# Performance work log

Measured on AMD Instinct MI355X. Metric: run time of the kernel, lower is better.

The kernel has to match this reference:

```python
import jax, jax.numpy as jnp
import numpy as np

N = 20000      # nodes
K = 32         # avg degree
E = N * K      # edges
H = 128        # num_hidden
NV = 128       # num_V
NE = 128       # num_E
NH = 4         # num_heads (hard-coded in module)
D = H // NH    # per-head dim


def setup_inputs() -> dict:
    key = jax.random.key(0)
    ks = jax.random.split(key, 16)
    w = lambda k, shape: jax.random.normal(k, shape, jnp.float32) * 0.02
    return {
        "h_V": jax.random.normal(ks[0], (N, NV), jnp.float32),
        "h_E": jax.random.normal(ks[1], (E, NE), jnp.float32),
        "edge_idx": jax.random.randint(ks[2], (2, E), 0, N, dtype=jnp.int64),
        # W_V: Linear(num_E, num_hidden) + GELU
        "Wv_w": w(ks[3], (H, NE)), "Wv_b": jnp.zeros((H,), jnp.float32),
        # Bias MLP: Linear(2*num_V+num_E, H) -> ReLU -> Linear(H, H) -> ReLU -> Linear(H, NH)
        "B1_w": w(ks[4], (H, 2 * NV + NE)), "B1_b": jnp.zeros((H,), jnp.float32),
        "B2_w": w(ks[5], (H, H)), "B2_b": jnp.zeros((H,), jnp.float32),
        "B3_w": w(ks[6], (NH, H)), "B3_b": jnp.zeros((NH,), jnp.float32),
        # W_O: Linear(H, num_V, bias=False); gate: Linear(H, num_V)
        "Wo_w": w(ks[7], (NV, H)),
        "gate_w": w(ks[8], (NV, H)), "gate_b": jnp.zeros((NV,), jnp.float32),
    }


def reference(h_V, h_E, edge_idx, Wv_w, Wv_b, B1_w, B1_b, B2_w, B2_b, B3_w, B3_b, Wo_w, gate_w, gate_b):
    src = edge_idx[0]
    dst = edge_idx[1]
    num_nodes = h_V.shape[0]

    # per-edge attention logits via small MLP on [h_V[src], h_E, h_V[dst]]
    cat = jnp.concatenate([h_V[src], h_E, h_V[dst]], axis=-1)          # [E, 2*NV+NE]
    x = jax.nn.relu(cat @ B1_w.T + B1_b)
    x = jax.nn.relu(x @ B2_w.T + B2_b)
    logits = (x @ B3_w.T + B3_b) / np.float32(np.sqrt(D))              # [E, NH]

    # per-edge values
    V = jax.nn.gelu(h_E @ Wv_w.T + Wv_b, approximate=False)           # [E, H]
    V = V.reshape(-1, NH, D)                                           # [E, NH, D]

    # scatter_softmax over edges grouped by src node
    m = jax.ops.segment_max(logits, src, num_segments=num_nodes)       # [N, NH]
    ex = jnp.exp(logits - m[src])                                      # [E, NH]
    denom = jax.ops.segment_sum(ex, src, num_segments=num_nodes)      # [N, NH]
    attend = ex / denom[src]                                           # [E, NH]

    # weighted scatter-sum aggregation
    agg = jax.ops.segment_sum(attend[:, :, None] * V, src, num_segments=num_nodes)
    agg = agg.reshape(num_nodes, -1)                                   # [N, H]

    h_V_gate = jax.nn.sigmoid(agg @ gate_w.T + gate_b)                 # [N, NV]
    dh = (agg @ Wo_w.T) * h_V_gate                                     # [N, NV]
    return h_V + dh
```

## Files before the change

### kernel.cpp

```cpp
#include <hip/hip_runtime.h>
#include <math.h>

typedef __attribute__((ext_vector_type(8))) short bf16x8;
typedef __attribute__((ext_vector_type(4))) float f32x4;
typedef unsigned short u16;

__device__ __forceinline__ short f2bf(float x) {
  union { float f; unsigned u; } c; c.f = x;
  unsigned u = c.u;
  u += 0x7fffu + ((u >> 16) & 1u);
  return (short)(u >> 16);
}
__device__ __forceinline__ float bf2f(u16 b) {
  union { unsigned u; float f; } c; c.u = ((unsigned)b) << 16; return c.f;
}
__device__ __forceinline__ unsigned pack2(float a, float b) {
  return ((unsigned)(u16)f2bf(a)) | (((unsigned)(u16)f2bf(b)) << 16);
}
__device__ __forceinline__ unsigned cvtpk(float lo, float hi) {
  unsigned r;
  asm("v_cvt_pk_bf16_f32 %0, %1, %2" : "=v"(r) : "v"(lo), "v"(hi));
  return r;
}
__device__ __forceinline__ float fast_erf(float x) {
  float ax = fabsf(x);
  float t = __frcp_rn(1.f + 0.3275911f * ax);
  float p = ((((1.061405429f * t - 1.453152027f) * t) + 1.421413741f) * t - 0.284496736f) * t + 0.254829592f;
  float y = 1.f - p * t * __expf(-ax * ax);
  return copysignf(y, x);
}
__device__ __forceinline__ void gload16(const void* g, void* l) {
  __builtin_amdgcn_global_load_lds(
      (const __attribute__((address_space(1))) void*)g,
      (__attribute__((address_space(3))) void*)l, 16, 0, 0);
}

__global__ void detect_kernel(const unsigned* __restrict__ idx32, int* __restrict__ flag) {
  __shared__ int anyNZ;
  if (threadIdx.x == 0) anyNZ = 0;
  __syncthreads();
  unsigned v = idx32[threadIdx.x * 2 + 1];
  if (v != 0u) atomicOr(&anyNZ, 1);
  __syncthreads();
  if (threadIdx.x == 0) *flag = (anyNZ == 0) ? 1 : 0;
}

__global__ void convert_count_kernel(const void* __restrict__ in, int* __restrict__ s32,
                                     const int* __restrict__ flag, int* __restrict__ cnt,
                                     int E) {
  int i = blockIdx.x * 256 + threadIdx.x;
  if (i >= 2 * E) return;
  int f = *flag;
  int v = f ? (int)((const long long*)in)[i] : ((const int*)in)[i];
  s32[i] = v;
  if (i < E) atomicAdd(&cnt[v], 1);
}

__global__ void __launch_bounds__(1024)
scan_kernel(const int* __restrict__ cnt, int* __restrict__ offs, int n) {
  __shared__ int sp[1024];
  int t = threadIdx.x;
  int chunk = (n + 1023) / 1024;
  int begin = t * chunk;
  int end = begin + chunk; if (end > n) end = n; if (begin > n) begin = n;
  int s = 0;
  for (int i = begin; i < end; ++i) s += cnt[i];
  sp[t] = s;
  __syncthreads();
  for (int o = 1; o < 1024; o <<= 1) {
    int v = (t >= o) ? sp[t - o] : 0;
    __syncthreads();
    sp[t] += v;
    __syncthreads();
  }
  int run = (t == 0) ? 0 : sp[t - 1];
  for (int i = begin; i < end; ++i) { offs[i] = run; run += cnt[i]; }
  if (t == 0) offs[n] = sp[1023];
}

__global__ void scatter_kernel(const int* __restrict__ src, const int* __restrict__ offs,
                               int* __restrict__ cur, int* __restrict__ order, int E) {
  int i = blockIdx.x * 256 + threadIdx.x;
  if (i >= E) return;
  int s = src[i];
  int p = offs[s] + atomicAdd(&cur[s], 1);
  order[p] = i;
}

__global__ void wcvt_kernel(const float* __restrict__ B1, const float* __restrict__ B2,
                            const float* __restrict__ B3, const float* __restrict__ Wv,
                            const float* __restrict__ Wo, const float* __restrict__ Wg,
                            short* __restrict__ o) {
  int i = blockIdx.x * 256 + threadIdx.x;
  if (i >= 115200) return;
  float val; int dst;
  if (i < 49152) {
    int row = i / 384, k = i % 384;
    val = B1[i];
    int c = k >> 5, s = (k >> 3) & 3, e = k & 7;
    dst = c * 4096 + row * 32 + ((s ^ ((row >> 1) & 3)) << 3) + e;
  } else if (i < 65536) {
    int j = i - 49152; int row = j >> 7, k = j & 127;
    val = B2[j];
    int c = k >> 5, s = (k >> 3) & 3, e = k & 7;
    dst = 49152 + c * 4096 + row * 32 + ((s ^ ((row >> 1) & 3)) << 3) + e;
  } else if (i < 66048) { val = B3[i - 65536]; dst = i; }
  else if (i < 82432) {
    int j = i - 66048; int row = j >> 7, k = j & 127;
    val = Wv[j];
    int c = k >> 5, s = (k >> 3) & 3, e = k & 7;
    dst = 66048 + c * 4096 + row * 32 + ((s ^ ((row >> 1) & 3)) << 3) + e;
  }
  else if (i < 98816)  { val = Wo[i - 82432]; dst = i; }
  else                 { val = Wg[i - 98816]; dst = i; }
  o[dst] = f2bf(val);
}

__global__ void cvtbf_kernel(const float* __restrict__ in, u16* __restrict__ out, long n8) {
  long i = (long)blockIdx.x * blockDim.x + threadIdx.x;
  long stride = (long)gridDim.x * blockDim.x;
  for (; i < n8; i += stride) {
    long b = i * 8;
    float4 a = *(const float4*)(in + b);
    float4 c = *(const float4*)(in + b + 4);
    uint4 u;
    u.x = pack2(a.x, a.y); u.y = pack2(a.z, a.w);
    u.z = pack2(c.x, c.y); u.w = pack2(c.z, c.w);
    *(uint4*)(out + b) = u;
  }
}

__global__ void __launch_bounds__(256, 3)
edge_kernel(const u16* __restrict__ hVb, const float* __restrict__ hE,
            const int* __restrict__ src, const int* __restrict__ dst,
            u16* __restrict__ Vout,
            const short* __restrict__ W1, const float* __restrict__ b1,
            const short* __restrict__ W2, const float* __restrict__ b2,
            const short* __restrict__ W3b, const float* __restrict__ b3,
            const short* __restrict__ Wv, const float* __restrict__ bv,
            float* __restrict__ logits, int E) {
  __shared__ u16 sE[64 * 128];
  __shared__ u16 sH[64 * 128];
  __shared__ u16 sW[2][4096];
  __shared__ float sPart[64][4][2];

  const int t = threadIdx.x;
  const int eBase = blockIdx.x * 64;
  const int lane = t & 63;
  const int wid = t >> 6;
  const int wrow = (wid >> 1) * 32;
  const int wcol = (wid & 1) * 64;
  const int lrow = lane & 15;
  const int kgrp = lane >> 4;

  auto STAGE = [&](const short* cp, int buf) {
#pragma unroll
    for (int i = 0; i < 2; ++i) {
      int L = t + i * 256;
      gload16(cp + L * 8, &sW[buf][L * 8]);
    }
  };

  STAGE(W1, 0);

#pragma unroll
  for (int i = 0; i < 4; ++i) {
    int u = t + i * 256;
    int row = u >> 4, sg = u & 15;
    const float* p = hE + (size_t)min(eBase + row, E - 1) * 128 + sg * 8;
    float4 f0 = *(const float4*)p;
    float4 f1 = *(const float4*)(p + 4);
    uint4 cv;
    cv.x = cvtpk(f0.x, f0.y); cv.y = cvtpk(f0.z, f0.w);
    cv.z = cvtpk(f1.x, f1.y); cv.w = cvtpk(f1.z, f1.w);
    *(uint4*)&sE[row * 128 + ((sg ^ (row & 15)) * 8)] = cv;
  }

  bf16x8 aS[4][2], aD[4][2];
  {
    int rS[2], rD[2];
#pragma unroll
    for (int mi = 0; mi < 2; ++mi) {
      int e = min(eBase + wrow + mi * 16 + lrow, E - 1);
      rS[mi] = src[e];
      rD[mi] = dst[e];
    }
#pragma unroll
    for (int c4 = 0; c4 < 4; ++c4) {
      const int kk = c4 * 32 + kgrp * 8;
#pragma unroll
      for (int mi = 0; mi < 2; ++mi) {
        aS[c4][mi] = *(const bf16x8*)(hVb + (size_t)rS[mi] * 128 + kk);
        aD[c4][mi] = *(const bf16x8*)(hVb + (size_t)rD[mi] * 128 + kk);
      }
    }
  }
  asm volatile("s_waitcnt vmcnt(0)" ::: "memory");
  __syncthreads();

  f32x4 acc[2][4];
  auto ZACC = [&]() {
#pragma unroll
    for (int mi = 0; mi < 2; ++mi)
#pragma unroll
      for (int nf = 0; nf < 4; ++nf)
#pragma unroll
        for (int q = 0; q < 4; ++q) acc[mi][nf][q] = 0.f;
  };
  auto LDSA = [&](const u16* s, int kk, bf16x8* a) {
#pragma unroll
    for (int mi = 0; mi < 2; ++mi) {
      int row = wrow + mi * 16 + lrow;
      int seg = (kk >> 3) ^ (row & 15);
      a[mi] = *(const bf16x8*)&s[row * 128 + seg * 8];
    }
  };
  auto STEP = [&](int buf, const short* nextCp, const bf16x8* a) {
    if (nextCp) STAGE(nextCp, buf ^ 1);
    bf16x8 b[4];
#pragma unroll
    for (int nf = 0; nf < 4; ++nf) {
      int row = wcol + nf * 16 + lrow;
      int seg = kgrp ^ ((row >> 1) & 3);
      b[nf] = *(const bf16x8*)&sW[buf][row * 32 + seg * 8];
    }
#pragma unroll
    for (int nf = 0; nf < 4; ++nf)
#pragma unroll
      for (int mi = 0; mi < 2; ++mi)
        acc[mi][nf] = __builtin_amdgcn_mfma_f32_16x16x32_bf16(a[mi], b[nf], acc[mi][nf], 0, 0, 0);
    if (nextCp) asm volatile("s_waitcnt vmcnt(0)" ::: "memory");
    __syncthreads();
  };

  ZACC();
  STEP(0, W1 + 1 * 4096, aS[0]);
  STEP(1, W1 + 2 * 4096, aS[1]);
  STEP(0, W1 + 3 * 4096, aS[2]);
  STEP(1, W1 + 4 * 4096, aS[3]);
#pragma unroll
  for (int c4 = 0; c4 < 4; ++c4) {
    bf16x8 a[2];
    LDSA(sE, c4 * 32 + kgrp * 8, a);
    STEP((4 + c4) & 1, W1 + (5 + c4) * 4096, a);
  }
  STEP(0, W1 + 9 * 4096, aD[0]);
  STEP(1, W1 + 10 * 4096, aD[1]);
  STEP(0, W1 + 11 * 4096, aD[2]);
  STEP(1, Wv, aD[3]);
  {
    float b1c[4];
#pragma unroll
    for (int nf = 0; nf < 4; ++nf) b1c[nf] = b1[wcol + nf * 16 + lrow];
#pragma unroll
    for (int mi = 0; mi < 2; ++mi)
#pragma unroll
      for (int nf = 0; nf < 4; ++nf)
#pragma unroll
        for (int q = 0; q < 4; ++q) {
          int row = wrow + mi * 16 + kgrp * 4 + q;
          int col = wcol + nf * 16 + lrow;
          int seg = (col >> 3) ^ (row & 15);
          sH[row * 128 + seg * 8 + (col & 7)] =
              (u16)f2bf(fmaxf(acc[mi][nf][q] + b1c[nf], 0.f));
        }
  }

  ZACC();
#pragma unroll
  for (int v = 0; v < 4; ++v) {
    bf16x8 a[2];
    LDSA(sE, v * 32 + kgrp * 8, a);
    const short* nxt = (v < 3) ? (Wv + (v + 1) * 4096) : W2;
    STEP(v & 1, nxt, a);
  }
  {
    float bvc[4];
#pragma unroll
    for (int nf = 0; nf < 4; ++nf) bvc[nf] = bv[wcol + nf * 16 + lrow];
#pragma unroll
    for (int mi = 0; mi < 2; ++mi)
#pragma unroll
      for (int nf = 0; nf < 4; ++nf)
#pragma unroll
        for (int q = 0; q < 4; ++q) {
          int row = wrow + mi * 16 + kgrp * 4 + q;
          int col = wcol + nf * 16 + lrow;
          float x = acc[mi][nf][q] + bvc[nf];
          float g = 0.5f * x * (1.0f + fast_erf(x * 0.70710678118654752f));
          int seg = (col >> 3) ^ (row & 15);
          sE[row * 128 + seg * 8 + (col & 7)] = (u16)f2bf(g);
        }
  }
  __syncthreads();
#pragma unroll
  for (int i = 0; i < 4; ++i) {
    int u = t + i * 256;
    int row = u >> 4, g16 = u & 15;
    int seg = g16 ^ (row & 15);
    uint4 v = *(const uint4*)&sE[row * 128 + seg * 8];
    int e = eBase + row;
    if (e < E) *(uint4*)(Vout + (size_t)e * 128 + g16 * 8) = v;
  }

  ZACC();
#pragma unroll
  for (int u = 0; u < 4; ++u) {
    bf16x8 a[2];
    LDSA(sH, u * 32 + kgrp * 8, a);
    const short* nxt = (u < 3) ? (W2 + (u + 1) * 4096) : nullptr;
    STEP(u & 1, nxt, a);
  }
  {
    float b2c[4], w3v[4][4];
#pragma unroll
    for (int nf = 0; nf < 4; ++nf) {
      int col = wcol + nf * 16 + lrow;
      b2c[nf] = b2[col];
#pragma unroll
      for (int h = 0; h < 4; ++h) w3v[h][nf] = bf2f((u16)W3b[h * 128 + col]);
    }
#pragma unroll
    for (int mi = 0; mi < 2; ++mi)
#pragma unroll
      for (int q = 0; q < 4; ++q) {
        float p0 = 0.f, p1 = 0.f, p2 = 0.f, p3 = 0.f;
#pragma unroll
        for (int nf = 0; nf < 4; ++nf) {
          float x = fmaxf(acc[mi][nf][q] + b2c[nf], 0.f);
          p0 += x * w3v[0][nf]; p1 += x * w3v[1][nf];
          p2 += x * w3v[2][nf]; p3 += x * w3v[3][nf];
        }
#pragma unroll
        for (int o = 1; o < 16; o <<= 1) {
          p0 += __shfl_xor(p0, o); p1 += __shfl_xor(p1, o);
          p2 += __shfl_xor(p2, o); p3 += __shfl_xor(p3, o);
        }
        if (lrow < 4) {
          float pw = (lrow == 0) ? p0 : (lrow == 1) ? p1 : (lrow == 2) ? p2 : p3;
          sPart[wrow + mi * 16 + kgrp * 4 + q][lrow][wid & 1] = pw;
        }
      }
  }
  __syncthreads();
  if (t < 64) {
    int e = eBase + t;
    if (e < E) {
      float4 lg;
      lg.x = (sPart[t][0][0] + sPart[t][0][1] + b3[0]) * 0.17677669529663687f;
      lg.y = (sPart[t][1][0] + sPart[t][1][1] + b3[1]) * 0.17677669529663687f;
      lg.z = (sPart[t][2][0] + sPart[t][2][1] + b3[2]) * 0.17677669529663687f;
      lg.w = (sPart[t][3][0] + sPart[t][3][1] + b3[3]) * 0.17677669529663687f;
      *(float4*)(logits + (size_t)e * 4) = lg;
    }
  }
}

__global__ void __launch_bounds__(256)
nm_kernel(const float* __restrict__ logits, const int* __restrict__ offs,
          const int* __restrict__ order, float* __restrict__ attw,
          float* __restrict__ inv, int nN) {
  const int wid = threadIdx.x >> 6, lane = threadIdx.x & 63;
  const int nW = gridDim.x * 4;
  for (int v = blockIdx.x * 4 + wid; v < nN; v += nW) {
    const int base = offs[v];
    const int deg = offs[v + 1] - base;
    float m0 = -3e38f, m1 = -3e38f, m2 = -3e38f, m3 = -3e38f;
    for (int i = lane; i < deg; i += 64) {
      int e = order[base + i];
      float4 l = *(const float4*)(logits + (size_t)e * 4);
      m0 = fmaxf(m0, l.x); m1 = fmaxf(m1, l.y);
      m2 = fmaxf(m2, l.z); m3 = fmaxf(m3, l.w);
    }
#pragma unroll
    for (int o = 32; o > 0; o >>= 1) {
      m0 = fmaxf(m0, __shfl_xor(m0, o)); m1 = fmaxf(m1, __shfl_xor(m1, o));
      m2 = fmaxf(m2, __shfl_xor(m2, o)); m3 = fmaxf(m3, __shfl_xor(m3, o));
    }
    float d0 = 0.f, d1 = 0.f, d2 = 0.f, d3 = 0.f;
    for (int i = lane; i < deg; i += 64) {
      int e = order[base + i];
      float4 l = *(const float4*)(logits + (size_t)e * 4);
      float4 ex;
      ex.x = __expf(l.x - m0); ex.y = __expf(l.y - m1);
      ex.z = __expf(l.z - m2); ex.w = __expf(l.w - m3);
      *(float4*)(attw + (size_t)e * 4) = ex;
      d0 += ex.x; d1 += ex.y; d2 += ex.z; d3 += ex.w;
    }
#pragma unroll
    for (int o = 32; o > 0; o >>= 1) {
      d0 += __shfl_xor(d0, o); d1 += __shfl_xor(d1, o);
      d2 += __shfl_xor(d2, o); d3 += __shfl_xor(d3, o);
    }
    if (lane < 4) {
      float dv = (lane == 0) ? d0 : (lane == 1) ? d1 : (lane == 2) ? d2 : d3;
      inv[(size_t)v * 4 + lane] = (dv > 0.f) ? 1.f / dv : 0.f;
    }
  }
}

__device__ __forceinline__ float dot8(const float* ag, uint4 w) {
  unsigned wr[4] = {w.x, w.y, w.z, w.w};
  float s = 0.f;
#pragma unroll
  for (int q = 0; q < 4; ++q) {
    s += ag[2 * q]     * bf2f((u16)(wr[q] & 0xffffu));
    s += ag[2 * q + 1] * bf2f((u16)(wr[q] >> 16));
  }
  return s;
}

__global__ void __launch_bounds__(256, 2)
agg_kernel(const float* __restrict__ hV, const float* __restrict__ attw,
           const float* __restrict__ inv, const u16* __restrict__ V,
           const int* __restrict__ offs, const int* __restrict__ order,
           const short* __restrict__ Wob, const short* __restrict__ Wgb,
           const float* __restrict__ gb, float* __restrict__ out, int nN) {
  __shared__ u16 sW[2][16384];
  __shared__ float sAgg[4][132];
  const int t = threadIdx.x;
#pragma unroll
  for (int i = 0; i < 8; ++i) {
    int idx = t + i * 256;
    int row = idx >> 4, k16 = idx & 15;
    int di = row * 128 + ((k16 ^ (row & 15)) * 8);
    *(uint4*)&sW[0][di] = ((const uint4*)Wob)[idx];
    *(uint4*)&sW[1][di] = ((const uint4*)Wgb)[idx];
  }
  __syncthreads();
  const int wid = t >> 6, lane = t & 63;
  const int dgrp = lane & 15, egrp = lane >> 4, h = dgrp >> 2;
  const int j0 = lane, j1 = lane + 64;
  const int s0 = (j0 & 15), s1 = (j1 & 15);
  for (int v = blockIdx.x * 4 + wid; v < nN; v += gridDim.x * 4) {
    const int base = offs[v], deg = offs[v + 1] - base;
    float a[8];
#pragma unroll
    for (int q = 0; q < 8; ++q) a[q] = 0.f;
    for (int i = egrp; i < deg; i += 4) {
      int e = order[base + i];
      float w = attw[(size_t)e * 4 + h];
      bf16x8 vv = *(const bf16x8*)(V + (size_t)e * 128 + dgrp * 8);
#pragma unroll
      for (int q = 0; q < 8; ++q) a[q] += w * bf2f((u16)vv[q]);
    }
#pragma unroll
    for (int q = 0; q < 8; ++q) {
      a[q] += __shfl_xor(a[q], 16);
      a[q] += __shfl_xor(a[q], 32);
    }
    if (egrp == 0) {
      float innv = inv[(size_t)v * 4 + h];
#pragma unroll
      for (int q = 0; q < 8; ++q) sAgg[wid][dgrp * 8 + q] = a[q] * innv;
    }
    asm volatile("s_waitcnt lgkmcnt(0)" ::: "memory");
    __builtin_amdgcn_wave_barrier();
    float o0 = 0.f, o1 = 0.f, g0 = 0.f, g1 = 0.f;
#pragma unroll 4
    for (int k = 0; k < 128; k += 8) {
      float a8[8];
#pragma unroll
      for (int q = 0; q < 8; ++q) a8[q] = sAgg[wid][k + q];
      int k16 = k >> 3;
      uint4 wo0 = *(const uint4*)&sW[0][j0 * 128 + ((k16 ^ s0) * 8)];
      uint4 wo1 = *(const uint4*)&sW[0][j1 * 128 + ((k16 ^ s1) * 8)];
      uint4 wg0 = *(const uint4*)&sW[1][j0 * 128 + ((k16 ^ s0) * 8)];
      uint4 wg1 = *(const uint4*)&sW[1][j1 * 128 + ((k16 ^ s1) * 8)];
      o0 += dot8(a8, wo0); o1 += dot8(a8, wo1);
      g0 += dot8(a8, wg0); g1 += dot8(a8, wg1);
    }
    float gg0 = 1.f / (1.f + __expf(-(g0 + gb[j0])));
    float gg1 = 1.f / (1.f + __expf(-(g1 + gb[j1])));
    out[(size_t)v * 128 + j0] = hV[(size_t)v * 128 + j0] + o0 * gg0;
    out[(size_t)v * 128 + j1] = hV[(size_t)v * 128 + j1] + o1 * gg1;
    asm volatile("s_waitcnt lgkmcnt(0)" ::: "memory");
    __builtin_amdgcn_wave_barrier();
  }
}

__global__ void fb_kernel(const float* __restrict__ hV, float* __restrict__ out, int n) {
  int i = blockIdx.x * 256 + threadIdx.x;
  if (i < n) out[i] = hV[i] + 0.5f;
}

extern "C" void kernel_launch(void* const* d_in, const int* in_sizes, int n_in,
                              void* d_out, int out_size, void* d_ws, size_t ws_size,
                              hipStream_t stream) {
  const float* hV   = (const float*)d_in[0];
  const float* hE   = (const float*)d_in[1];
  const void*  eidx = d_in[2];
  const float* WvW  = (const float*)d_in[3];
  const float* WvB  = (const float*)d_in[4];
  const float* B1w  = (const float*)d_in[5];
  const float* B1b  = (const float*)d_in[6];
  const float* B2w  = (const float*)d_in[7];
  const float* B2b  = (const float*)d_in[8];
  const float* B3w  = (const float*)d_in[9];
  const float* B3b  = (const float*)d_in[10];
  const float* WoW  = (const float*)d_in[11];
  const float* GW   = (const float*)d_in[12];
  const float* GB   = (const float*)d_in[13];

  const int Nn = in_sizes[0] / 128;
  const int E  = in_sizes[1] / 128;
  if (Nn <= 0 || E <= 0) return;

  char* ws = (char*)d_ws;
  size_t off = 0;
  auto alloc = [&](size_t b) { size_t o = off; off += (b + 255) & ~(size_t)255; return o; };
  const size_t o_idx   = alloc((size_t)2 * E * 4);
  const size_t o_cnt   = alloc((size_t)(Nn + 1) * 4);
  const size_t o_offs  = alloc((size_t)(Nn + 1) * 4);
  const size_t o_cur   = alloc((size_t)Nn * 4);
  const size_t o_order = alloc((size_t)E * 4);
  const size_t o_flag  = alloc(256);
  const size_t o_log   = alloc((size_t)E * 16);
  const size_t o_attw  = alloc((size_t)E * 16);
  const size_t o_inv   = alloc((size_t)Nn * 16);
  const size_t o_V     = alloc((size_t)E * 256);
  const size_t o_hVb   = alloc((size_t)Nn * 256);
  const size_t o_wbf   = alloc((size_t)115200 * 2);

  if (off > ws_size) {
    fb_kernel<<<(out_size + 255) / 256, 256, 0, stream>>>(hV, (float*)d_out, out_size);
    return;
  }

  int*   idx32  = (int*)(ws + o_idx);
  int*   cnt    = (int*)(ws + o_cnt);
  int*   offsP  = (int*)(ws + o_offs);
  int*   cur    = (int*)(ws + o_cur);
  int*   order  = (int*)(ws + o_order);
  int*   flag   = (int*)(ws + o_flag);
  float* logits = (float*)(ws + o_log);
  float* attw   = (float*)(ws + o_attw);
  float* invd   = (float*)(ws + o_inv);
  u16*   Vb     = (u16*)(ws + o_V);
  u16*   hVb    = (u16*)(ws + o_hVb);
  short* wbf    = (short*)(ws + o_wbf);

  short* W1b = wbf;
  short* W2b = wbf + 49152;
  short* W3b = wbf + 65536;
  short* Wvb = wbf + 66048;
  short* Wob = wbf + 82432;
  short* Wgb = wbf + 98816;

  const int* src = idx32;
  const int* dst = idx32 + E;

  detect_kernel<<<1, 256, 0, stream>>>((const unsigned*)eidx, flag);
  hipMemsetAsync(cnt, 0, (size_t)(Nn + 1) * 4, stream);
  hipMemsetAsync(cur, 0, (size_t)Nn * 4, stream);
  convert_count_kernel<<<(2 * E + 255) / 256, 256, 0, stream>>>(eidx, idx32, flag, cnt, E);
  scan_kernel<<<1, 1024, 0, stream>>>(cnt, offsP, Nn);
  scatter_kernel<<<(E + 255) / 256, 256, 0, stream>>>(src, offsP, cur, order, E);
  wcvt_kernel<<<(115200 + 255) / 256, 256, 0, stream>>>(B1w, B2w, B3w, WvW, WoW, GW, wbf);
  cvtbf_kernel<<<512, 256, 0, stream>>>(hV, hVb, (long)Nn * 16);

  edge_kernel<<<(E + 63) / 64, 256, 0, stream>>>(
      hVb, hE, src, dst, Vb, W1b, B1b, W2b, B2b, W3b, B3b, Wvb, WvB, logits, E);

  nm_kernel<<<2048, 256, 0, stream>>>(logits, offsP, order, attw, invd, Nn);

  agg_kernel<<<512, 256, 0, stream>>>(
      hV, attw, invd, Vb, offsP, order, Wob, Wgb, GB, (float*)d_out, Nn);
}
```

Before: 557.8 us.

## Merge edge-kernel LDS buffers, reorder GEMMs, and use cheaper erf approximation

The edge kernel now computes the W_V GEMM first and keeps its pre-activation results packed as bf16 in registers. This lets one 64x128 LDS tile serve as h_E input, then hidden activations, then GELU output, cutting shared memory so occupancy can rise from 3 to 4 blocks per SM. The erf approximation switches from an exp-based form to a rational polynomial with one reciprocal, and bf16 conversion uses the hardware pack instruction. Risks are higher register pressure from holding the packed values across the later GEMMs, plus lower accuracy in both erf and the pre-GELU values, which are now rounded to bf16 before the activation.

New measurement: 629.0 us. +12.8%, slower.

```diff
diff --git a/kernel.cpp b/kernel.cpp
--- a/kernel.cpp
+++ b/kernel.cpp
@@ -22,12 +22,24 @@
   asm("v_cvt_pk_bf16_f32 %0, %1, %2" : "=v"(r) : "v"(lo), "v"(hi));
   return r;
 }
+__device__ __forceinline__ u16 f2bf1(float x) {
+  return (u16)cvtpk(x, x);
+}
+__device__ __forceinline__ float bfu_lo(unsigned v) {
+  union { unsigned u; float f; } c; c.u = v << 16; return c.f;
+}
+__device__ __forceinline__ float bfu_hi(unsigned v) {
+  union { unsigned u; float f; } c; c.u = v & 0xffff0000u; return c.f;
+}
 __device__ __forceinline__ float fast_erf(float x) {
   float ax = fabsf(x);
-  float t = __frcp_rn(1.f + 0.3275911f * ax);
-  float p = ((((1.061405429f * t - 1.453152027f) * t) + 1.421413741f) * t - 0.284496736f) * t + 0.254829592f;
-  float y = 1.f - p * t * __expf(-ax * ax);
+  float p = 1.f + ax * (0.278393f + ax * (0.230389f + ax * (0.000972f + ax * 0.078108f)));
+  p = p * p; p = p * p;
+  float y = 1.f - __frcp_rn(p);
   return copysignf(y, x);
+}
+__device__ __forceinline__ float gelu1(float x) {
+  return 0.5f * x * (1.0f + fast_erf(x * 0.70710678118654752f));
 }
 __device__ __forceinline__ void gload16(const void* g, void* l) {
   __builtin_amdgcn_global_load_lds(
@@ -130,7 +142,7 @@
   }
 }
 
-__global__ void __launch_bounds__(256, 3)
+__global__ void __launch_bounds__(256, 4)
 edge_kernel(const u16* __restrict__ hVb, const float* __restrict__ hE,
             const int* __restrict__ src, const int* __restrict__ dst,
             u16* __restrict__ Vout,
@@ -139,8 +151,7 @@
             const short* __restrict__ W3b, const float* __restrict__ b3,
             const short* __restrict__ Wv, const float* __restrict__ bv,
             float* __restrict__ logits, int E) {
-  __shared__ u16 sE[64 * 128];
-  __shared__ u16 sH[64 * 128];
+  __shared__ u16 sEH[64 * 128];
   __shared__ u16 sW[2][4096];
   __shared__ float sPart[64][4][2];
 
@@ -161,7 +172,7 @@
     }
   };
 
-  STAGE(W1, 0);
+  STAGE(Wv, 0);
 
 #pragma unroll
   for (int i = 0; i < 4; ++i) {
@@ -173,7 +184,7 @@
     uint4 cv;
     cv.x = cvtpk(f0.x, f0.y); cv.y = cvtpk(f0.z, f0.w);
     cv.z = cvtpk(f1.x, f1.y); cv.w = cvtpk(f1.z, f1.w);
-    *(uint4*)&sE[row * 128 + ((sg ^ (row & 15)) * 8)] = cv;
+    *(uint4*)&sEH[row * 128 + ((sg ^ (row & 15)) * 8)] = cv;
   }
 
   bf16x8 aS[4][2], aD[4][2];
@@ -207,12 +218,12 @@
 #pragma unroll
         for (int q = 0; q < 4; ++q) acc[mi][nf][q] = 0.f;
   };
-  auto LDSA = [&](const u16* s, int kk, bf16x8* a) {
+  auto LDSA = [&](int kk, bf16x8* a) {
 #pragma unroll
     for (int mi = 0; mi < 2; ++mi) {
       int row = wrow + mi * 16 + lrow;
       int seg = (kk >> 3) ^ (row & 15);
-      a[mi] = *(const bf16x8*)&s[row * 128 + seg * 8];
+      a[mi] = *(const bf16x8*)&sEH[row * 128 + seg * 8];
     }
   };
   auto STEP = [&](int buf, const short* nextCp, const bf16x8* a) {
@@ -234,20 +245,44 @@
   };
 
   ZACC();
+#pragma unroll
+  for (int c = 0; c < 4; ++c) {
+    bf16x8 a[2];
+    LDSA(c * 32 + kgrp * 8, a);
+    const short* nxt = (c < 3) ? (Wv + (c + 1) * 4096) : (W1 + 4 * 4096);
+    STEP(c & 1, nxt, a);
+  }
+  unsigned vpk[2][4][2];
+  {
+    float bvc[4];
+#pragma unroll
+    for (int nf = 0; nf < 4; ++nf) bvc[nf] = bv[wcol + nf * 16 + lrow];
+#pragma unroll
+    for (int mi = 0; mi < 2; ++mi)
+#pragma unroll
+      for (int nf = 0; nf < 4; ++nf) {
+        vpk[mi][nf][0] = cvtpk(acc[mi][nf][0] + bvc[nf], acc[mi][nf][1] + bvc[nf]);
+        vpk[mi][nf][1] = cvtpk(acc[mi][nf][2] + bvc[nf], acc[mi][nf][3] + bvc[nf]);
+      }
+  }
+
+  ZACC();
+#pragma unroll
+  for (int c = 0; c < 4; ++c) {
+    bf16x8 a[2];
+    LDSA(c * 32 + kgrp * 8, a);
+    const short* nxt = (c < 3) ? (W1 + (5 + c) * 4096) : W1;
+    STEP(c & 1, nxt, a);
+  }
   STEP(0, W1 + 1 * 4096, aS[0]);
   STEP(1, W1 + 2 * 4096, aS[1]);
   STEP(0, W1 + 3 * 4096, aS[2]);
-  STEP(1, W1 + 4 * 4096, aS[3]);
-#pragma unroll
-  for (int c4 = 0; c4 < 4; ++c4) {
-    bf16x8 a[2];
-    LDSA(sE, c4 * 32 + kgrp * 8, a);
-    STEP((4 + c4) & 1, W1 + (5 + c4) * 4096, a);
-  }
+  STEP(1, W1 + 8 * 4096, aS[3]);
   STEP(0, W1 + 9 * 4096, aD[0]);
   STEP(1, W1 + 10 * 4096, aD[1]);
   STEP(0, W1 + 11 * 4096, aD[2]);
-  STEP(1, Wv, aD[3]);
+  STEP(1, W2, aD[3]);
+
   {
     float b1c[4];
 #pragma unroll
@@ -261,55 +296,19 @@
           int row = wrow + mi * 16 + kgrp * 4 + q;
           int col = wcol + nf * 16 + lrow;
           int seg = (col >> 3) ^ (row & 15);
-          sH[row * 128 + seg * 8 + (col & 7)] =
-              (u16)f2bf(fmaxf(acc[mi][nf][q] + b1c[nf], 0.f));
+          sEH[row * 128 + seg * 8 + (col & 7)] =
+              f2bf1(fmaxf(acc[mi][nf][q] + b1c[nf], 0.f));
         }
   }
+  __syncthreads();
 
   ZACC();
 #pragma unroll
-  for (int v = 0; v < 4; ++v) {
+  for (int c = 0; c < 4; ++c) {
     bf16x8 a[2];
-    LDSA(sE, v * 32 + kgrp * 8, a);
-    const short* nxt = (v < 3) ? (Wv + (v + 1) * 4096) : W2;
-    STEP(v & 1, nxt, a);
-  }
-  {
-    float bvc[4];
-#pragma unroll
-    for (int nf = 0; nf < 4; ++nf) bvc[nf] = bv[wcol + nf * 16 + lrow];
-#pragma unroll
-    for (int mi = 0; mi < 2; ++mi)
-#pragma unroll
-      for (int nf = 0; nf < 4; ++nf)
-#pragma unroll
-        for (int q = 0; q < 4; ++q) {
-          int row = wrow + mi * 16 + kgrp * 4 + q;
-          int col = wcol + nf * 16 + lrow;
-          float x = acc[mi][nf][q] + bvc[nf];
-          float g = 0.5f * x * (1.0f + fast_erf(x * 0.70710678118654752f));
-          int seg = (col >> 3) ^ (row & 15);
-          sE[row * 128 + seg * 8 + (col & 7)] = (u16)f2bf(g);
-        }
-  }
-  __syncthreads();
-#pragma unroll
-  for (int i = 0; i < 4; ++i) {
-    int u = t + i * 256;
-    int row = u >> 4, g16 = u & 15;
-    int seg = g16 ^ (row & 15);
-    uint4 v = *(const uint4*)&sE[row * 128 + seg * 8];
-    int e = eBase + row;
-    if (e < E) *(uint4*)(Vout + (size_t)e * 128 + g16 * 8) = v;
-  }
-
-  ZACC();
-#pragma unroll
-  for (int u = 0; u < 4; ++u) {
-    bf16x8 a[2];
-    LDSA(sH, u * 32 + kgrp * 8, a);
-    const short* nxt = (u < 3) ? (W2 + (u + 1) * 4096) : nullptr;
-    STEP(u & 1, nxt, a);
+    LDSA(c * 32 + kgrp * 8, a);
+    const short* nxt = (c < 3) ? (W2 + (c + 1) * 4096) : nullptr;
+    STEP(c & 1, nxt, a);
   }
   {
     float b2c[4], w3v[4][4];
@@ -353,6 +352,32 @@
       lg.w = (sPart[t][3][0] + sPart[t][3][1] + b3[3]) * 0.17677669529663687f;
       *(float4*)(logits + (size_t)e * 4) = lg;
     }
+  }
+
+#pragma unroll
+  for (int mi = 0; mi < 2; ++mi)
+#pragma unroll
+    for (int nf = 0; nf < 4; ++nf)
+#pragma unroll
+      for (int p = 0; p < 2; ++p) {
+        float x0 = bfu_lo(vpk[mi][nf][p]);
+        float x1 = bfu_hi(vpk[mi][nf][p]);
+        int col = wcol + nf * 16 + lrow;
+        int row0 = wrow + mi * 16 + kgrp * 4 + p * 2;
+        int seg0 = (col >> 3) ^ (row0 & 15);
+        int seg1 = (col >> 3) ^ ((row0 + 1) & 15);
+        sEH[row0 * 128 + seg0 * 8 + (col & 7)] = f2bf1(gelu1(x0));
+        sEH[(row0 + 1) * 128 + seg1 * 8 + (col & 7)] = f2bf1(gelu1(x1));
+      }
+  __syncthreads();
+#pragma unroll
+  for (int i = 0; i < 4; ++i) {
+    int u = t + i * 256;
+    int row = u >> 4, g16 = u & 15;
+    int seg = g16 ^ (row & 15);
+    uint4 v = *(const uint4*)&sEH[row * 128 + seg * 8];
+    int e = eBase + row;
+    if (e < E) *(uint4*)(Vout + (size_t)e * 128 + g16 * 8) = v;
   }
 }
 
```
